# Kernel optimization log

Hardware: AMD Instinct MI355X
Metric: run time of the kernel (lower is better)

Reference implementation:

```python
import jax, jax.numpy as jnp
import numpy as np

BS = 4096
D = 256
TAU = 0.5
EPS = 1e-08          # eps added to negative-sum denominator (module arg)
COS_EPS = 1e-08      # nn.CosineSimilarity norm clamp


def setup_inputs() -> dict:
    key = jax.random.key(0)
    k1, k2 = jax.random.split(key)
    zi = jax.random.normal(k1, (BS, D), dtype=jnp.float32)
    zj = jax.random.normal(k2, (BS, D), dtype=jnp.float32)
    return {"zi": zi, "zj": zj}


def reference(zi, zj):
    bs = zi.shape[0]
    n = 2 * bs
    z = jnp.concatenate([zi, zj], axis=0)                       # [2bs, D]
    # cosine similarity = normalized dot products (norms clamped like torch)
    norm = jnp.linalg.norm(z, axis=-1, keepdims=True)
    zn = z / jnp.maximum(norm, COS_EPS)
    sim = jnp.matmul(zn, zn.T) / TAU                            # [2bs, 2bs]
    e = jnp.exp(sim)
    # positive pairs: row i pairs with column (i+bs) mod 2bs
    rows = jnp.arange(n)
    pair = jnp.concatenate([jnp.arange(bs) + bs, jnp.arange(bs)])
    sim_pos = e[rows, pair]                                     # [2bs]
    # negatives: all entries in a row except the diagonal
    sim_neg_sum = e.sum(axis=-1) - jnp.diagonal(e)              # [2bs]
    loss = jnp.mean(-jnp.log(sim_pos / (sim_neg_sum + EPS)))
    return loss
```

## Files before the change

### kernel.cpp

```cpp
#include <hip/hip_runtime.h>
#include <hip/hip_bf16.h>


#define N_ROWS 8192
#define BSZ    4096
#define DIM    256
#define INV_TAU 2.0f
#define EPS_REF 1e-8f
#define COS_EPS 1e-8f
#define NG2     64
#define NTILES  (NG2 * (NG2 + 1) / 2)
#define LSTRIDE 260

typedef __attribute__((ext_vector_type(4))) float f32x4;
typedef __attribute__((ext_vector_type(8))) int   v8i;
typedef union { int4 x[2]; v8i v; } frag32;

__device__ __forceinline__ float red16(float x) {
    x += __int_as_float(__builtin_amdgcn_update_dpp(0, __float_as_int(x), 0x121, 0xf, 0xf, false));
    x += __int_as_float(__builtin_amdgcn_update_dpp(0, __float_as_int(x), 0x122, 0xf, 0xf, false));
    x += __int_as_float(__builtin_amdgcn_update_dpp(0, __float_as_int(x), 0x124, 0xf, 0xf, false));
    x += __int_as_float(__builtin_amdgcn_update_dpp(0, __float_as_int(x), 0x128, 0xf, 0xf, false));
    return x;
}

__global__ __launch_bounds__(256) void knorm(const float* __restrict__ zi,
                                             const float* __restrict__ zj,
                                             unsigned char* __restrict__ znsw,
                                             float* __restrict__ out) {
    __shared__ float lds[16 * LSTRIDE];
    __shared__ float nrm[16];
    const int rg = blockIdx.x;
    const int t  = threadIdx.x;
    const int w  = t >> 6;
    const int l  = t & 63;
    const int row0 = rg * 16;
    if (rg == 0 && t == 0) out[0] = 0.f;

    #pragma unroll
    for (int s = 0; s < 4; ++s) {
        const int row = s * 4 + w;
        const int r   = row0 + row;
        const float* src = (r < BSZ) ? zi + (size_t)r * DIM + l * 4
                                     : zj + (size_t)(r - BSZ) * DIM + l * 4;
        const float4 v = *(const float4*)src;
        *(float4*)&lds[row * LSTRIDE + l * 4] = v;
        float ss = v.x*v.x + v.y*v.y + v.z*v.z + v.w*v.w;
        #pragma unroll
        for (int off = 32; off >= 1; off >>= 1) ss += __shfl_xor(ss, off);
        if (l == 0) nrm[row] = 1.0f / fmaxf(sqrtf(ss), COS_EPS);
    }
    __syncthreads();

    const int pi = t >> 6, fl = t & 63;
    const int h = pi >> 1, p = pi & 1;
    const int r16 = fl & 15, q = fl >> 4;
    const int k0 = h * 128 + q * 32 + p * 16;
    const float inv = nrm[r16];
    float f[16];
    #pragma unroll
    for (int j = 0; j < 16; ++j) f[j] = lds[r16 * LSTRIDE + k0 + j] * inv;
    int wd[4];
    #pragma unroll
    for (int g = 0; g < 4; ++g) {
        int a = 0;
        a = __builtin_amdgcn_cvt_pk_fp8_f32(f[g*4+0], f[g*4+1], a, false);
        a = __builtin_amdgcn_cvt_pk_fp8_f32(f[g*4+2], f[g*4+3], a, true);
        wd[g] = a;
    }
    *(int4*)(znsw + (size_t)rg * 4096 + pi * 1024 + fl * 16) =
        make_int4(wd[0], wd[1], wd[2], wd[3]);
}

__global__ __launch_bounds__(256, 3) void kgemm(const unsigned char* __restrict__ znsw,
                                                float* __restrict__ P,
                                                float* __restrict__ selfdot,
                                                float* __restrict__ pairdot) {
    __shared__ __align__(16) unsigned char pan[32768];
    const int w = threadIdx.x >> 6;
    const int l = threadIdx.x & 63;

    const int t = blockIdx.x;
    int Gi = (int)((129.0f - sqrtf(16641.0f - 8.0f * (float)t)) * 0.5f);
    while ((Gi + 1) * (129 - (Gi + 1)) / 2 <= t) ++Gi;
    while (Gi * (129 - Gi) / 2 > t) --Gi;
    const int Gj = Gi + (t - Gi * (129 - Gi) / 2);

    const char* srcA = (const char*)znsw + (size_t)Gi * 32768;
    #pragma unroll
    for (int sub = 0; sub < 8; ++sub) {
        const int off = sub * 4096 + w * 1024;
        __builtin_amdgcn_global_load_lds(
            (const __attribute__((address_space(1))) void*)(srcA + off + l * 16),
            (__attribute__((address_space(3))) void*)(&pan[off]), 16, 0, 0);
    }

    const int rh = w >> 1, ch = w & 1;
    const char* bbase = (const char*)znsw + (size_t)Gj * 32768 + ch * 4 * 4096 + l * 16;

    frag32 B0[4], B1[4];
    #pragma unroll
    for (int nt = 0; nt < 4; ++nt) {
        B0[nt].x[0] = *(const int4*)(bbase + nt * 4096);
        B0[nt].x[1] = *(const int4*)(bbase + nt * 4096 + 1024);
        B1[nt].x[0] = *(const int4*)(bbase + nt * 4096 + 2048);
        B1[nt].x[1] = *(const int4*)(bbase + nt * 4096 + 3072);
    }

    f32x4 acc[4][4];
    #pragma unroll
    for (int mt = 0; mt < 4; ++mt)
        #pragma unroll
        for (int nt = 0; nt < 4; ++nt)
            acc[mt][nt] = (f32x4){0.f, 0.f, 0.f, 0.f};

    __syncthreads();

    #pragma unroll
    for (int h = 0; h < 2; ++h)
        #pragma unroll
        for (int mt = 0; mt < 4; ++mt) {
            frag32 A;
            const char* ap = (const char*)&pan[(rh * 4 + mt) * 4096 + h * 2048] + l * 16;
            A.x[0] = *(const int4*)(ap);
            A.x[1] = *(const int4*)(ap + 1024);
            #pragma unroll
            for (int nt = 0; nt < 4; ++nt) {
                const v8i bv = (h == 0) ? B0[nt].v : B1[nt].v;
                acc[mt][nt] = __builtin_amdgcn_mfma_scale_f32_16x16x128_f8f6f4(
                    A.v, bv, acc[mt][nt],
                    0, 0,
                    0, 0x7f7f7f7f,
                    0, 0x7f7f7f7f);
            }
        }

    const int c = l & 15, q = l >> 4;
    const int rsel = c - 4 * q;
    const bool vld = (rsel >= 0) && (rsel < 4);

    if ((Gi == Gj || Gj == Gi + 32) && rh == ch) {
        float dv[4];
        #pragma unroll
        for (int mt = 0; mt < 4; ++mt) {
            float d = acc[mt][mt][0];
            #pragma unroll
            for (int r = 1; r < 4; ++r)
                if (rsel == r) d = acc[mt][mt][r];
            dv[mt] = d;
        }
        if (vld) {
            float* dst = (Gi == Gj) ? selfdot : pairdot;
            #pragma unroll
            for (int mt = 0; mt < 4; ++mt)
                dst[Gi * 128 + rh * 64 + mt * 16 + c] = dv[mt];
        }
    }

    #pragma unroll
    for (int mt = 0; mt < 4; ++mt)
        #pragma unroll
        for (int nt = 0; nt < 4; ++nt)
            #pragma unroll
            for (int r = 0; r < 4; ++r)
                acc[mt][nt][r] = __expf(acc[mt][nt][r] * INV_TAU);

    float rs[4][4];
    #pragma unroll
    for (int mt = 0; mt < 4; ++mt)
        #pragma unroll
        for (int r = 0; r < 4; ++r)
            rs[mt][r] = red16(acc[mt][0][r] + acc[mt][1][r] + acc[mt][2][r] + acc[mt][3][r]);
    if (c == 0) {
        #pragma unroll
        for (int mt = 0; mt < 4; ++mt) {
            const f32x4 o4 = (f32x4){rs[mt][0], rs[mt][1], rs[mt][2], rs[mt][3]};
            __builtin_nontemporal_store(o4,
                (f32x4*)&P[(size_t)(Gj * 2 + ch) * N_ROWS + Gi * 128 + rh * 64 + mt * 16 + q * 4]);
        }
    }

    if (Gi != Gj) {
        float cs[4];
        #pragma unroll
        for (int nt = 0; nt < 4; ++nt) {
            float s = 0.f;
            #pragma unroll
            for (int mt = 0; mt < 4; ++mt)
                #pragma unroll
                for (int r = 0; r < 4; ++r)
                    s += acc[mt][nt][r];
            s += __shfl_xor(s, 16);
            s += __shfl_xor(s, 32);
            cs[nt] = s;
        }
        if (q == 0) {
            #pragma unroll
            for (int nt = 0; nt < 4; ++nt)
                __builtin_nontemporal_store(cs[nt],
                    &P[(size_t)(Gi * 2 + rh) * N_ROWS + Gj * 128 + ch * 64 + nt * 16 + c]);
        }
    }
}

__global__ __launch_bounds__(256) void kfinal(const float* __restrict__ P,
                                              const float* __restrict__ selfdot,
                                              const float* __restrict__ pairdot,
                                              float* __restrict__ out) {
    const int l = threadIdx.x & 63;
    const int w = threadIdx.x >> 6;
    const int row = blockIdx.x * 64 + l;
    float s = 0.f;
    #pragma unroll
    for (int st = 0; st < 32; ++st)
        s += P[(size_t)(w * 32 + st) * N_ROWS + row];
    __shared__ float wsum[4][64];
    wsum[w][l] = s;
    __syncthreads();
    if (w == 0) {
        const float tot = wsum[0][l] + wsum[1][l] + wsum[2][l] + wsum[3][l];
        const float selfe = __expf(selfdot[row] * INV_TAU);
        const float pd    = pairdot[(row < BSZ) ? row : row - BSZ];
        float loss = logf(tot - selfe + EPS_REF) - pd * INV_TAU;
        #pragma unroll
        for (int off = 32; off >= 1; off >>= 1) loss += __shfl_xor(loss, off);
        if (l == 0) atomicAdd(out, loss * (1.0f / (float)N_ROWS));
    }
}

extern "C" void kernel_launch(void* const* d_in, const int* in_sizes, int n_in,
                              void* d_out, int out_size, void* d_ws, size_t ws_size,
                              hipStream_t stream) {
    const float* zi = (const float*)d_in[0];
    const float* zj = (const float*)d_in[1];
    float* out = (float*)d_out;

    char* ws = (char*)d_ws;
    unsigned char* znsw = (unsigned char*)ws;
    float* P       = (float*)(ws + 2 * 1024 * 1024);
    float* selfdot = (float*)(ws + 6 * 1024 * 1024);
    float* pairdot = (float*)(ws + 6 * 1024 * 1024 + 32 * 1024);

    knorm <<<N_ROWS / 16, 256, 0, stream>>>(zi, zj, znsw, out);
    kgemm <<<NTILES, 256, 0, stream>>>(znsw, P, selfdot, pairdot);
    kfinal<<<N_ROWS / 64, 256, 0, stream>>>(P, selfdot, pairdot, out);
}
```

Before: 83.13 us.

## Process up to four column tiles per block reusing the LDS A panel

Each kgemm block now loads its row panel into LDS once and loops over up to four consecutive column tiles of the upper triangle, cutting the grid from 2080 to 544 blocks. This removes repeated A-panel global loads and per-block launch and sync overhead. In exchange each block runs serially longer with fewer blocks to fill the CUs, the last group per row is partial, and B fragments are now loaded per half inside the loop.

```diff
diff --git a/kernel.cpp b/kernel.cpp
--- a/kernel.cpp
+++ b/kernel.cpp
@@ -9,7 +9,7 @@
 #define EPS_REF 1e-8f
 #define COS_EPS 1e-8f
 #define NG2     64
-#define NTILES  (NG2 * (NG2 + 1) / 2)
+#define NBLK    544
 #define LSTRIDE 260
 
 typedef __attribute__((ext_vector_type(4))) float f32x4;
@@ -80,11 +80,11 @@
     const int w = threadIdx.x >> 6;
     const int l = threadIdx.x & 63;
 
-    const int t = blockIdx.x;
-    int Gi = (int)((129.0f - sqrtf(16641.0f - 8.0f * (float)t)) * 0.5f);
-    while ((Gi + 1) * (129 - (Gi + 1)) / 2 <= t) ++Gi;
-    while (Gi * (129 - Gi) / 2 > t) --Gi;
-    const int Gj = Gi + (t - Gi * (129 - Gi) / 2);
+    int t  = blockIdx.x;
+    int Gi = 0;
+    int cnt = 16;
+    while (t >= cnt) { t -= cnt; ++Gi; cnt = (64 - Gi + 3) >> 2; }
+    const int Gj0 = Gi + t * 4;
 
     const char* srcA = (const char*)znsw + (size_t)Gi * 32768;
     #pragma unroll
@@ -96,109 +96,110 @@
     }
 
     const int rh = w >> 1, ch = w & 1;
-    const char* bbase = (const char*)znsw + (size_t)Gj * 32768 + ch * 4 * 4096 + l * 16;
-
-    frag32 B0[4], B1[4];
-    #pragma unroll
-    for (int nt = 0; nt < 4; ++nt) {
-        B0[nt].x[0] = *(const int4*)(bbase + nt * 4096);
-        B0[nt].x[1] = *(const int4*)(bbase + nt * 4096 + 1024);
-        B1[nt].x[0] = *(const int4*)(bbase + nt * 4096 + 2048);
-        B1[nt].x[1] = *(const int4*)(bbase + nt * 4096 + 3072);
-    }
-
-    f32x4 acc[4][4];
-    #pragma unroll
-    for (int mt = 0; mt < 4; ++mt)
-        #pragma unroll
-        for (int nt = 0; nt < 4; ++nt)
-            acc[mt][nt] = (f32x4){0.f, 0.f, 0.f, 0.f};
-
-    __syncthreads();
-
-    #pragma unroll
-    for (int h = 0; h < 2; ++h)
-        #pragma unroll
-        for (int mt = 0; mt < 4; ++mt) {
-            frag32 A;
-            const char* ap = (const char*)&pan[(rh * 4 + mt) * 4096 + h * 2048] + l * 16;
-            A.x[0] = *(const int4*)(ap);
-            A.x[1] = *(const int4*)(ap + 1024);
-            #pragma unroll
-            for (int nt = 0; nt < 4; ++nt) {
-                const v8i bv = (h == 0) ? B0[nt].v : B1[nt].v;
-                acc[mt][nt] = __builtin_amdgcn_mfma_scale_f32_16x16x128_f8f6f4(
-                    A.v, bv, acc[mt][nt],
-                    0, 0,
-                    0, 0x7f7f7f7f,
-                    0, 0x7f7f7f7f);
-            }
-        }
-
     const int c = l & 15, q = l >> 4;
     const int rsel = c - 4 * q;
     const bool vld = (rsel >= 0) && (rsel < 4);
 
-    if ((Gi == Gj || Gj == Gi + 32) && rh == ch) {
-        float dv[4];
-        #pragma unroll
-        for (int mt = 0; mt < 4; ++mt) {
-            float d = acc[mt][mt][0];
-            #pragma unroll
-            for (int r = 1; r < 4; ++r)
-                if (rsel == r) d = acc[mt][mt][r];
-            dv[mt] = d;
-        }
-        if (vld) {
-            float* dst = (Gi == Gj) ? selfdot : pairdot;
-            #pragma unroll
-            for (int mt = 0; mt < 4; ++mt)
-                dst[Gi * 128 + rh * 64 + mt * 16 + c] = dv[mt];
-        }
-    }
-
-    #pragma unroll
-    for (int mt = 0; mt < 4; ++mt)
-        #pragma unroll
-        for (int nt = 0; nt < 4; ++nt)
+    __syncthreads();
+
+    for (int jj = 0; jj < 4; ++jj) {
+        const int Gj = Gj0 + jj;
+        if (Gj > 63) break;
+
+        const char* bbase = (const char*)znsw + (size_t)Gj * 32768 + ch * 16384 + l * 16;
+
+        f32x4 acc[4][4];
+        #pragma unroll
+        for (int mt = 0; mt < 4; ++mt)
+            #pragma unroll
+            for (int nt = 0; nt < 4; ++nt)
+                acc[mt][nt] = (f32x4){0.f, 0.f, 0.f, 0.f};
+
+        #pragma unroll
+        for (int h = 0; h < 2; ++h) {
+            frag32 B[4];
+            #pragma unroll
+            for (int nt = 0; nt < 4; ++nt) {
+                B[nt].x[0] = *(const int4*)(bbase + nt * 4096 + h * 2048);
+                B[nt].x[1] = *(const int4*)(bbase + nt * 4096 + h * 2048 + 1024);
+            }
+            #pragma unroll
+            for (int mt = 0; mt < 4; ++mt) {
+                frag32 A;
+                const char* ap = (const char*)&pan[(rh * 4 + mt) * 4096 + h * 2048] + l * 16;
+                A.x[0] = *(const int4*)(ap);
+                A.x[1] = *(const int4*)(ap + 1024);
+                #pragma unroll
+                for (int nt = 0; nt < 4; ++nt)
+                    acc[mt][nt] = __builtin_amdgcn_mfma_scale_f32_16x16x128_f8f6f4(
+                        A.v, B[nt].v, acc[mt][nt],
+                        0, 0,
+                        0, 0x7f7f7f7f,
+                        0, 0x7f7f7f7f);
+            }
+        }
+
+        if ((Gi == Gj || Gj == Gi + 32) && rh == ch) {
+            float dv[4];
+            #pragma unroll
+            for (int mt = 0; mt < 4; ++mt) {
+                float d = acc[mt][mt][0];
+                #pragma unroll
+                for (int r = 1; r < 4; ++r)
+                    if (rsel == r) d = acc[mt][mt][r];
+                dv[mt] = d;
+            }
+            if (vld) {
+                float* dst = (Gi == Gj) ? selfdot : pairdot;
+                #pragma unroll
+                for (int mt = 0; mt < 4; ++mt)
+                    dst[Gi * 128 + rh * 64 + mt * 16 + c] = dv[mt];
+            }
+        }
+
+        #pragma unroll
+        for (int mt = 0; mt < 4; ++mt)
+            #pragma unroll
+            for (int nt = 0; nt < 4; ++nt)
+                #pragma unroll
+                for (int r = 0; r < 4; ++r)
+                    acc[mt][nt][r] = __expf(acc[mt][nt][r] * INV_TAU);
+
+        float rs[4][4];
+        #pragma unroll
+        for (int mt = 0; mt < 4; ++mt)
             #pragma unroll
             for (int r = 0; r < 4; ++r)
-                acc[mt][nt][r] = __expf(acc[mt][nt][r] * INV_TAU);
-
-    float rs[4][4];
-    #pragma unroll
-    for (int mt = 0; mt < 4; ++mt)
-        #pragma unroll
-        for (int r = 0; r < 4; ++r)
-            rs[mt][r] = red16(acc[mt][0][r] + acc[mt][1][r] + acc[mt][2][r] + acc[mt][3][r]);
-    if (c == 0) {
-        #pragma unroll
-        for (int mt = 0; mt < 4; ++mt) {
-            const f32x4 o4 = (f32x4){rs[mt][0], rs[mt][1], rs[mt][2], rs[mt][3]};
-            __builtin_nontemporal_store(o4,
-                (f32x4*)&P[(size_t)(Gj * 2 + ch) * N_ROWS + Gi * 128 + rh * 64 + mt * 16 + q * 4]);
-        }
-    }
-
-    if (Gi != Gj) {
-        float cs[4];
-        #pragma unroll
-        for (int nt = 0; nt < 4; ++nt) {
-            float s = 0.f;
-            #pragma unroll
-            for (int mt = 0; mt < 4; ++mt)
-                #pragma unroll
-                for (int r = 0; r < 4; ++r)
-                    s += acc[mt][nt][r];
-            s += __shfl_xor(s, 16);
-            s += __shfl_xor(s, 32);
-            cs[nt] = s;
-        }
-        if (q == 0) {
-            #pragma unroll
-            for (int nt = 0; nt < 4; ++nt)
-                __builtin_nontemporal_store(cs[nt],
-                    &P[(size_t)(Gi * 2 + rh) * N_ROWS + Gj * 128 + ch * 64 + nt * 16 + c]);
+                rs[mt][r] = red16(acc[mt][0][r] + acc[mt][1][r] + acc[mt][2][r] + acc[mt][3][r]);
+        if (c == 0) {
+            #pragma unroll
+            for (int mt = 0; mt < 4; ++mt) {
+                const f32x4 o4 = (f32x4){rs[mt][0], rs[mt][1], rs[mt][2], rs[mt][3]};
+                __builtin_nontemporal_store(o4,
+                    (f32x4*)&P[(size_t)(Gj * 2 + ch) * N_ROWS + Gi * 128 + rh * 64 + mt * 16 + q * 4]);
+            }
+        }
+
+        if (Gi != Gj) {
+            float cs[4];
+            #pragma unroll
+            for (int nt = 0; nt < 4; ++nt) {
+                float s = 0.f;
+                #pragma unroll
+                for (int mt = 0; mt < 4; ++mt)
+                    #pragma unroll
+                    for (int r = 0; r < 4; ++r)
+                        s += acc[mt][nt][r];
+                s += __shfl_xor(s, 16);
+                s += __shfl_xor(s, 32);
+                cs[nt] = s;
+            }
+            if (q == 0) {
+                #pragma unroll
+                for (int nt = 0; nt < 4; ++nt)
+                    __builtin_nontemporal_store(cs[nt],
+                        &P[(size_t)(Gi * 2 + rh) * N_ROWS + Gj * 128 + ch * 64 + nt * 16 + c]);
+            }
         }
     }
 }
@@ -242,6 +243,6 @@
     float* pairdot = (float*)(ws + 6 * 1024 * 1024 + 32 * 1024);
 
     knorm <<<N_ROWS / 16, 256, 0, stream>>>(zi, zj, znsw, out);
-    kgemm <<<NTILES, 256, 0, stream>>>(znsw, P, selfdot, pairdot);
+    kgemm <<<NBLK, 256, 0, stream>>>(znsw, P, selfdot, pairdot);
     kfinal<<<N_ROWS / 64, 256, 0, stream>>>(P, selfdot, pairdot, out);
 }
```

After: 86.03 us. +3.5%, slower.
